# Optimization experiments

Measured on AMD Instinct MI355X. Metric: run time of the kernel, lower is better.

Reference implementation:

```python
import jax, jax.numpy as jnp
import numpy as np

ANCHOR_N = 5
W_POS = 5.0     # weight for position loss (YOLO lambda_coord)
W_NOOBJ = 0.5   # weight for no-object confidence loss (YOLO lambda_noobj)
EPS = 1e-8


def _split(x, a_n):
    # x: [N, C, H, W] -> (position [N,H,W,A,4], conf [N,H,W,A,1], scores [N,H,W,A,K-5])
    N, C, H, W = x.shape
    K = C // a_n
    x = x.reshape(N, a_n, K, H, W).transpose(0, 3, 4, 1, 2)  # N,H,W,A,K
    return x[..., 0:4], x[..., 4:5], x[..., 5:]


def _iou(a, b):
    # a: [N,H,W,A,4], b: [N,H,W,1,4], boxes as (x1,y1,x2,y2) -> iou [N,H,W,A]
    lt = jnp.maximum(a[..., :2], b[..., :2])
    rb = jnp.minimum(a[..., 2:], b[..., 2:])
    wh = jnp.clip(rb - lt, 0.0)
    inter = wh[..., 0] * wh[..., 1]
    area_a = jnp.clip(a[..., 2] - a[..., 0], 0.0) * jnp.clip(a[..., 3] - a[..., 1], 0.0)
    area_b = jnp.clip(b[..., 2] - b[..., 0], 0.0) * jnp.clip(b[..., 3] - b[..., 1], 0.0)
    return inter / (area_a + area_b - inter + EPS)


def setup_inputs() -> dict:
    key = jax.random.key(0)
    k1, k2 = jax.random.split(key)
    N, C, H, W = 64, 425, 52, 52  # C = ANCHOR_N * (5 + 80 classes)
    out = jax.random.normal(k1, (N, C, H, W), dtype=jnp.float32)
    gt = jax.random.normal(k2, (N, C, H, W), dtype=jnp.float32)
    return {"out": out, "gt": gt}


def reference(out, gt):
    o_pos, o_conf, o_sc = _split(out, ANCHOR_N)
    g_pos, g_conf, g_sc = _split(gt, ANCHOR_N)
    dtype = out.dtype

    no_obj_mask = (g_conf == 0).astype(dtype)   # [N,H,W,A,1]
    has_obj_mask = (g_conf > 0).astype(dtype)   # [N,H,W,A,1]

    # Per-cell IoU of each predicted anchor box vs the cell's gt box (anchor 0 of gt),
    # vectorized replacement of the original triple N/H/W Python loop.
    iou = _iou(o_pos, g_pos[:, :, :, 0:1, :])              # [N,H,W,A]
    best = jnp.argmax(iou, axis=-1)                        # [N,H,W]
    resp = jax.nn.one_hot(best, ANCHOR_N, dtype=dtype)[..., None]  # [N,H,W,A,1]
    resp = resp * has_obj_mask                             # responsible anchor in object cells

    N = out.shape[0]
    iou_t = jax.lax.stop_gradient(iou)[..., None]          # conf target = iou (no grad)

    loss_pos = W_POS * jnp.sum(resp * (o_pos - g_pos) ** 2) / N
    loss_conf_obj = jnp.sum(resp * (o_conf - iou_t) ** 2) / N
    loss_conf_noobj = W_NOOBJ * jnp.sum(no_obj_mask * o_conf ** 2) / N
    loss_scores = jnp.sum(has_obj_mask * (o_sc - g_sc) ** 2) / N

    return loss_pos + loss_conf_obj + loss_conf_noobj + loss_scores
```

## Files before the change

kernel.cpp:

```cpp
#include <hip/hip_runtime.h>


#define A_N 5
#define KPA 85
#define N_BATCH 64
#define HW 2704
#define CSTRIDE 2704
#define NSTRIDE (425 * 2704)
#define N_CELLS (N_BATCH * HW)
#define WPOS 5.0f
#define WNOOBJ 0.5f
#define EPSF 1e-8f

__global__ __launch_bounds__(256) void yolo_loss_kernel(
    const float* __restrict__ out, const float* __restrict__ gt,
    float* __restrict__ loss)
{
    const int idx = blockIdx.x * blockDim.x + threadIdx.x;
    float acc = 0.0f;

    if (idx < N_CELLS) {
        const int n  = idx / HW;
        const int hw = idx - n * HW;
        const int base = n * NSTRIDE + hw;

        float gconf[A_N];
        bool anyObj = false, anyNoObj = false;
#pragma unroll
        for (int a = 0; a < A_N; ++a) {
            gconf[a] = gt[base + (a * KPA + 4) * CSTRIDE];
            anyObj   |= (gconf[a] > 0.0f);
            anyNoObj |= (gconf[a] == 0.0f);
        }

        if (anyNoObj) {
#pragma unroll
            for (int a = 0; a < A_N; ++a) {
                if (gconf[a] == 0.0f) {
                    float oc = out[base + (a * KPA + 4) * CSTRIDE];
                    acc += WNOOBJ * oc * oc;
                }
            }
        }

        if (anyObj) {
            float gb0, gb1, gb2, gb3;
            gb0 = gt[base + 0 * CSTRIDE];
            gb1 = gt[base + 1 * CSTRIDE];
            gb2 = gt[base + 2 * CSTRIDE];
            gb3 = gt[base + 3 * CSTRIDE];
            const float areaB = fmaxf(gb2 - gb0, 0.0f) * fmaxf(gb3 - gb1, 0.0f);

            float op[A_N][4];
            float iou[A_N];
#pragma unroll
            for (int a = 0; a < A_N; ++a) {
#pragma unroll
                for (int k = 0; k < 4; ++k)
                    op[a][k] = out[base + (a * KPA + k) * CSTRIDE];
                float ltx = fmaxf(op[a][0], gb0);
                float lty = fmaxf(op[a][1], gb1);
                float rbx = fminf(op[a][2], gb2);
                float rby = fminf(op[a][3], gb3);
                float w = fmaxf(rbx - ltx, 0.0f);
                float h = fmaxf(rby - lty, 0.0f);
                float inter = w * h;
                float areaA = fmaxf(op[a][2] - op[a][0], 0.0f) *
                              fmaxf(op[a][3] - op[a][1], 0.0f);
                iou[a] = inter / (areaA + areaB - inter + EPSF);
            }
            float best_iou = -1.0f;
            int best = 0;
#pragma unroll
            for (int a = 0; a < A_N; ++a) {
                if (iou[a] > best_iou) { best_iou = iou[a]; best = a; }
            }

            if (gconf[best] > 0.0f) {
                float lp = 0.0f;
#pragma unroll
                for (int k = 0; k < 4; ++k) {
                    float g = gt[base + (best * KPA + k) * CSTRIDE];
                    float d = op[best][k] - g;
                    lp += d * d;
                }
                acc += WPOS * lp;
                float oc = out[base + (best * KPA + 4) * CSTRIDE];
                float d = oc - best_iou;
                acc += d * d;
            }

#pragma unroll
            for (int a = 0; a < A_N; ++a) {
                if (gconf[a] > 0.0f) {
                    const int sb = base + (a * KPA + 5) * CSTRIDE;
                    float s = 0.0f;
#pragma unroll 8
                    for (int k = 0; k < 80; ++k) {
                        float d = out[sb + k * CSTRIDE] - gt[sb + k * CSTRIDE];
                        s = fmaf(d, d, s);
                    }
                    acc += s;
                }
            }
        }
    }

#pragma unroll
    for (int off = 32; off > 0; off >>= 1)
        acc += __shfl_down(acc, off);

    __shared__ float wsum[4];
    const int lane = threadIdx.x & 63;
    const int wid  = threadIdx.x >> 6;
    if (lane == 0) wsum[wid] = acc;
    __syncthreads();
    if (threadIdx.x == 0) {
        float s = (wsum[0] + wsum[1] + wsum[2] + wsum[3]) * (1.0f / N_BATCH);
        atomicAdd(loss, s);
    }
}

extern "C" void kernel_launch(void* const* d_in, const int* in_sizes, int n_in,
                              void* d_out, int out_size, void* d_ws, size_t ws_size,
                              hipStream_t stream) {
    const float* out_p = (const float*)d_in[0];
    const float* gt_p  = (const float*)d_in[1];
    float* loss = (float*)d_out;

    hipMemsetAsync(loss, 0, sizeof(float), stream);

    const int threads = 256;
    const int blocks = (N_CELLS + threads - 1) / threads;
    yolo_loss_kernel<<<blocks, threads, 0, stream>>>(out_p, gt_p, loss);
}
```

Before: 110.8 us.

## Split score loss into separate vectorized channel-parallel blocks

Class-score squared differences move out of the per-cell threads and into dedicated blocks. Each thread there handles two score channels for four adjacent cells and loops over the batch using float4 loads. The object mask is applied with a predicated select instead of a branch. This targets divergent, scalar, strided loads in the memory-bound score loop, at the cost of always reading every score value and re-reading the confidence channel.

After: 127.1 us. +14.7%, slower.

```diff
diff --git a/kernel.cpp b/kernel.cpp
--- a/kernel.cpp
+++ b/kernel.cpp
@@ -5,21 +5,29 @@
 #define KPA 85
 #define N_BATCH 64
 #define HW 2704
+#define Q4 (HW / 4)
 #define CSTRIDE 2704
 #define NSTRIDE (425 * 2704)
 #define N_CELLS (N_BATCH * HW)
+#define CTRL_BLOCKS 676
+#define N_SCORE_THREADS (Q4 * 200)
+#define SCORE_BLOCKS 529
 #define WPOS 5.0f
 #define WNOOBJ 0.5f
 #define EPSF 1e-8f
+
+__device__ __forceinline__ float4 ld4(const float* __restrict__ p, int elem_off) {
+    return *reinterpret_cast<const float4*>(p + elem_off);
+}
 
 __global__ __launch_bounds__(256) void yolo_loss_kernel(
     const float* __restrict__ out, const float* __restrict__ gt,
     float* __restrict__ loss)
 {
-    const int idx = blockIdx.x * blockDim.x + threadIdx.x;
     float acc = 0.0f;
 
-    if (idx < N_CELLS) {
+    if (blockIdx.x < CTRL_BLOCKS) {
+        const int idx = blockIdx.x * blockDim.x + threadIdx.x;
         const int n  = idx / HW;
         const int hw = idx - n * HW;
         const int base = n * NSTRIDE + hw;
@@ -44,11 +52,10 @@
         }
 
         if (anyObj) {
-            float gb0, gb1, gb2, gb3;
-            gb0 = gt[base + 0 * CSTRIDE];
-            gb1 = gt[base + 1 * CSTRIDE];
-            gb2 = gt[base + 2 * CSTRIDE];
-            gb3 = gt[base + 3 * CSTRIDE];
+            float gb0 = gt[base + 0 * CSTRIDE];
+            float gb1 = gt[base + 1 * CSTRIDE];
+            float gb2 = gt[base + 2 * CSTRIDE];
+            float gb3 = gt[base + 3 * CSTRIDE];
             const float areaB = fmaxf(gb2 - gb0, 0.0f) * fmaxf(gb3 - gb1, 0.0f);
 
             float op[A_N][4];
@@ -58,12 +65,8 @@
 #pragma unroll
                 for (int k = 0; k < 4; ++k)
                     op[a][k] = out[base + (a * KPA + k) * CSTRIDE];
-                float ltx = fmaxf(op[a][0], gb0);
-                float lty = fmaxf(op[a][1], gb1);
-                float rbx = fminf(op[a][2], gb2);
-                float rby = fminf(op[a][3], gb3);
-                float w = fmaxf(rbx - ltx, 0.0f);
-                float h = fmaxf(rby - lty, 0.0f);
+                float w = fmaxf(fminf(op[a][2], gb2) - fmaxf(op[a][0], gb0), 0.0f);
+                float h = fmaxf(fminf(op[a][3], gb3) - fmaxf(op[a][1], gb1), 0.0f);
                 float inter = w * h;
                 float areaA = fmaxf(op[a][2] - op[a][0], 0.0f) *
                               fmaxf(op[a][3] - op[a][1], 0.0f);
@@ -82,27 +85,46 @@
                 for (int k = 0; k < 4; ++k) {
                     float g = gt[base + (best * KPA + k) * CSTRIDE];
                     float d = op[best][k] - g;
-                    lp += d * d;
+                    lp = fmaf(d, d, lp);
                 }
                 acc += WPOS * lp;
                 float oc = out[base + (best * KPA + 4) * CSTRIDE];
                 float d = oc - best_iou;
                 acc += d * d;
             }
+        }
+    } else {
+        const int stid = (blockIdx.x - CTRL_BLOCKS) * blockDim.x + threadIdx.x;
+        if (stid < N_SCORE_THREADS) {
+            const int cpair = stid / Q4;
+            const int q     = stid - cpair * Q4;
+            const int a     = cpair / 40;
+            const int kk    = (cpair - a * 40) * 2;
+            const int e0 = (a * KPA + 5 + kk) * CSTRIDE + 4 * q;
+            const int e1 = e0 + CSTRIDE;
+            const int eg = (a * KPA + 4) * CSTRIDE + 4 * q;
 
-#pragma unroll
-            for (int a = 0; a < A_N; ++a) {
-                if (gconf[a] > 0.0f) {
-                    const int sb = base + (a * KPA + 5) * CSTRIDE;
-                    float s = 0.0f;
-#pragma unroll 8
-                    for (int k = 0; k < 80; ++k) {
-                        float d = out[sb + k * CSTRIDE] - gt[sb + k * CSTRIDE];
-                        s = fmaf(d, d, s);
-                    }
-                    acc += s;
-                }
+            float accA = 0.0f, accB = 0.0f;
+#pragma unroll 2
+            for (int n = 0; n < N_BATCH; ++n) {
+                const int b = n * NSTRIDE;
+                float4 o0 = ld4(out, b + e0);
+                float4 g0 = ld4(gt,  b + e0);
+                float4 o1 = ld4(out, b + e1);
+                float4 g1 = ld4(gt,  b + e1);
+                float4 gc = ld4(gt,  b + eg);
+
+                float d0, d1, s;
+                d0 = o0.x - g0.x; d1 = o1.x - g1.x; s = fmaf(d0, d0, d1 * d1);
+                accA += (gc.x > 0.0f) ? s : 0.0f;
+                d0 = o0.y - g0.y; d1 = o1.y - g1.y; s = fmaf(d0, d0, d1 * d1);
+                accB += (gc.y > 0.0f) ? s : 0.0f;
+                d0 = o0.z - g0.z; d1 = o1.z - g1.z; s = fmaf(d0, d0, d1 * d1);
+                accA += (gc.z > 0.0f) ? s : 0.0f;
+                d0 = o0.w - g0.w; d1 = o1.w - g1.w; s = fmaf(d0, d0, d1 * d1);
+                accB += (gc.w > 0.0f) ? s : 0.0f;
             }
+            acc = accA + accB;
         }
     }
 
@@ -130,7 +152,6 @@
 
     hipMemsetAsync(loss, 0, sizeof(float), stream);
 
-    const int threads = 256;
-    const int blocks = (N_CELLS + threads - 1) / threads;
-    yolo_loss_kernel<<<blocks, threads, 0, stream>>>(out_p, gt_p, loss);
+    const int blocks = CTRL_BLOCKS + SCORE_BLOCKS;
+    yolo_loss_kernel<<<blocks, 256, 0, stream>>>(out_p, gt_p, loss);
 }
```
